# Kernel tuning notes

Measured on AMD Instinct MI355X. Metric: run time of the kernel, lower is better.

Reference implementation:

```python
import jax, jax.numpy as jnp
import numpy as np

B, N = 16, 4096

def _fps(xyz, npoint):
    # iterative farthest point sampling on one cloud [n,3] -> [npoint] int32
    n = xyz.shape[0]
    def body(carry, _):
        dist, far = carry
        d = jnp.sum((xyz - xyz[far]) ** 2, axis=-1)
        dist = jnp.minimum(dist, d)
        return (dist, jnp.argmax(dist).astype(jnp.int32)), far
    _, idx = jax.lax.scan(body, (jnp.full((n,), 1e10, jnp.float32), jnp.int32(0)), None, length=npoint)
    return idx

def _ball_query(radius, nsample, xyz, new_xyz):
    # xyz [n,3], new_xyz [S,3] -> [S,nsample] neighbor indices (first-in-index order, as in PointNet++)
    n = xyz.shape[0]
    sqr = jnp.sum((new_xyz[:, None, :] - xyz[None, :, :]) ** 2, axis=-1)  # [S,n]
    idx = jnp.where(sqr > radius * radius, n, jnp.arange(n, dtype=jnp.int32)[None, :])
    idx = jnp.sort(idx, axis=-1)[:, :nsample]
    return jnp.where(idx == n, idx[:, :1], idx)

def _gather(p, i):
    return jax.vmap(lambda pp, ii: pp[ii])(p, i)

def _mlp(x, layers):
    # shared MLP = 1x1 conv over grouped points; BN(eval) folded into (W,b)
    for W, b in layers:
        x = jax.nn.relu(jnp.einsum('bsnc,co->bsno', x, W) + b)
    return x

def _sa(xyz, feats, npoint, radius, nsample, layers):
    fps_idx = jax.vmap(lambda p: _fps(p, npoint))(xyz)            # [B,S]
    new_xyz = _gather(xyz, fps_idx)                                # [B,S,3]
    idx = jax.vmap(lambda p, q: _ball_query(radius, nsample, p, q))(xyz, new_xyz)  # [B,S,ns]
    x = _gather(xyz, idx) - new_xyz[:, :, None, :]                 # centered grouped xyz
    if feats is not None:
        x = jnp.concatenate([x, _gather(feats, idx)], axis=-1)
    x = _mlp(x, layers)
    return new_xyz, jnp.max(x, axis=2)

def _forward(points, w10, b10, w11, b11, w12, b12, w20, b20, w21, b21, w22, b22, w30, b30, w31, b31, w32, b32, lw1, lb1, lw2, lb2, fw1, fb1, fw2, fb2, pos_mean, pos_std, rot_mean, rot_std):
    l1x, l1f = _sa(points, None, 512, 0.2, 32, [(w10, b10), (w11, b11), (w12, b12)])
    l2x, l2f = _sa(l1x, l1f, 128, 0.4, 64, [(w20, b20), (w21, b21), (w22, b22)])
    # sa3: group_all
    x = jnp.concatenate([l2x, l2f], axis=-1)[:, None]              # [B,1,128,259]
    x = _mlp(x, [(w30, b30), (w31, b31), (w32, b32)])
    g = jnp.max(x, axis=2).reshape(points.shape[0], 1024)
    label = jax.nn.sigmoid(jax.nn.relu(g @ lw1 + lb1) @ lw2 + lb2)  # dropout = identity (eval)
    res = jax.nn.relu(g @ fw1 + fb1) @ fw2 + fb2
    pl = res[:, 0:3] * pos_std + pos_mean
    rl = res[:, 3:9] * rot_std + rot_mean
    pr = res[:, 9:12] * pos_std + pos_mean
    rr = res[:, 12:18] * rot_std + rot_mean
    return jnp.concatenate([label, pl, rl, pr, rr], axis=-1)       # [B,20]

def setup_inputs():
    ks = iter(jax.random.split(jax.random.key(0), 64))
    def w(shape, s=0.05):
        return jax.random.normal(next(ks), shape, jnp.float32) * s
    inp = {'points': jax.random.normal(next(ks), (B, N, 3), jnp.float32) * 0.5}
    dims = {'w10': (3, 64), 'w11': (64, 64), 'w12': (64, 128), 'w20': (131, 128), 'w21': (128, 128), 'w22': (128, 256), 'w30': (259, 256), 'w31': (256, 512), 'w32': (512, 1024), 'lw1': (1024, 256), 'lw2': (256, 2), 'fw1': (1024, 512), 'fw2': (512, 18)}
    for name, s in dims.items():
        inp[name] = w(s)
        inp[name.replace('w', 'b', 1)] = jnp.zeros((s[1],), jnp.float32)
    inp['pos_mean'] = w((3,), 0.1)
    inp['pos_std'] = jnp.abs(w((3,))) + 1.0
    inp['rot_mean'] = w((6,), 0.1)
    inp['rot_std'] = jnp.abs(w((6,))) + 1.0
    return inp

def reference(points, w10, b10, w11, b11, w12, b12, w20, b20, w21, b21, w22, b22, w30, b30, w31, b31, w32, b32, lw1, lb1, lw2, lb2, fw1, fb1, fw2, fb2, pos_mean, pos_std, rot_mean, rot_std):
    return _forward(points, w10, b10, w11, b11, w12, b12, w20, b20, w21, b21, w22, b22, w30, b30, w31, b31, w32, b32, lw1, lb1, lw2, lb2, fw1, fb1, fw2, fb2, pos_mean, pos_std, rot_mean, rot_std)
```

## Files before the change

### kernel.cpp

```cpp
#include <hip/hip_runtime.h>
#include <math.h>

#define BB 16
#define NN 4096

typedef float v2f __attribute__((ext_vector_type(2)));

__device__ __forceinline__ v2f pkfma(v2f a, v2f b, v2f c) {
    return __builtin_elementwise_fma(a, b, c);
}

__device__ __forceinline__ float sq3(float dx, float dy, float dz) {
    return __fadd_rn(__fadd_rn(__fmul_rn(dx, dx), __fmul_rn(dy, dy)), __fmul_rn(dz, dz));
}

template<int CTRL, int RMASK>
__device__ __forceinline__ unsigned long long dpp_max_step(unsigned long long P) {
    int lo = __builtin_amdgcn_update_dpp(0, (int)(unsigned)P,        CTRL, RMASK, 0xf, true);
    int hi = __builtin_amdgcn_update_dpp(0, (int)(unsigned)(P >> 32), CTRL, RMASK, 0xf, true);
    unsigned long long o = ((unsigned long long)(unsigned)hi << 32) | (unsigned)lo;
    return (o > P) ? o : P;
}

__device__ __forceinline__ unsigned long long dpp_wave_max_u64(unsigned long long P) {
    P = dpp_max_step<0x111, 0xf>(P);
    P = dpp_max_step<0x112, 0xf>(P);
    P = dpp_max_step<0x114, 0xf>(P);
    P = dpp_max_step<0x118, 0xf>(P);
    P = dpp_max_step<0x142, 0xa>(P);
    P = dpp_max_step<0x143, 0xc>(P);
    return P;
}

__device__ __forceinline__ unsigned long long u64max(unsigned long long a, unsigned long long b) {
    return (a > b) ? a : b;
}

template<int NPTS, int NPOINT, int TPB>
__global__ __launch_bounds__(TPB) void fps_kernel(const float* __restrict__ xyz,
                                                  float* __restrict__ newxyz,
                                                  float* __restrict__ out_t,
                                                  int ts) {
    constexpr int PPT = NPTS / TPB;
    constexpr int NW  = TPB / 64;
    static_assert(NPOINT <= TPB, "far-history latch needs NPOINT <= TPB");
    __shared__ float sx[NPTS], sy[NPTS], sz[NPTS];
    __shared__ __align__(16) unsigned long long slot[2][NW];
    const int b = blockIdx.x;
    const int tid = threadIdx.x;
    const float* base = xyz + (size_t)b * NPTS * 3;
    for (int i = tid; i < NPTS; i += TPB) {
        sx[i] = base[i * 3 + 0];
        sy[i] = base[i * 3 + 1];
        sz[i] = base[i * 3 + 2];
    }
    __syncthreads();
    float px[PPT], py[PPT], pz[PPT], dist[PPT];
#pragma unroll
    for (int k = 0; k < PPT; k++) {
        int p = tid + k * TPB;
        px[k] = sx[p]; py[k] = sy[p]; pz[k] = sz[p];
        dist[k] = 1e10f;
    }
    int far = 0;
    int myfar = 0;
    const int lane = tid & 63, wid = tid >> 6;
    for (int it = 0; it < NPOINT; it++) {
        if (tid == it) myfar = far;
        float fx = sx[far], fy = sy[far], fz = sz[far];
        float bv = -1.0f; int bi = 0;
#pragma unroll
        for (int k = 0; k < PPT; k++) {
            float d = sq3(px[k] - fx, py[k] - fy, pz[k] - fz);
            float nd = fminf(dist[k], d);
            dist[k] = nd;
            if (nd > bv) { bv = nd; bi = tid + k * TPB; }
        }
        unsigned long long P = ((unsigned long long)__float_as_uint(bv) << 32)
                             | (unsigned long long)(~(unsigned)bi & 0xFFFFFFFFull);
        P = dpp_wave_max_u64(P);
        int bufi = it & 1;
        if (lane == 63) slot[bufi][wid] = P;
        __syncthreads();
        unsigned long long v[NW];
#pragma unroll
        for (int w = 0; w < NW; w++) v[w] = slot[bufi][w];
#pragma unroll
        for (int st = NW / 2; st >= 1; st >>= 1)
#pragma unroll
            for (int w = 0; w < st; w++) v[w] = u64max(v[w], v[w + st]);
        far = (int)(~(unsigned)(v[0] & 0xFFFFFFFFull));
    }
    if (tid < NPOINT) {
        float fx = sx[myfar], fy = sy[myfar], fz = sz[myfar];
        newxyz[((size_t)b * NPOINT + tid) * 3 + 0] = fx;
        newxyz[((size_t)b * NPOINT + tid) * 3 + 1] = fy;
        newxyz[((size_t)b * NPOINT + tid) * 3 + 2] = fz;
        if (out_t) {
            out_t[0 * ts + b * NPOINT + tid] = fx;
            out_t[1 * ts + b * NPOINT + tid] = fy;
            out_t[2 * ts + b * NPOINT + tid] = fz;
        }
    }
}

template<int NS>
__device__ __forceinline__ void bq_body(const float* __restrict__ pts, int n,
                                        const float* __restrict__ centers, int S,
                                        float r2, int* __restrict__ outidx,
                                        int wave, int lane) {
    int b = wave / S, s = wave % S;
    const float* c = centers + ((size_t)b * S + s) * 3;
    float cx = c[0], cy = c[1], cz = c[2];
    const float* pb = pts + (size_t)b * n * 3;
    int* out = outidx + ((size_t)b * S + s) * NS;
    int total = 0, first = -1;
    int rounds = n >> 6;
    for (int r = 0; r < rounds; r++) {
        int p = (r << 6) + lane;
        float dx = pb[p * 3 + 0] - cx, dy = pb[p * 3 + 1] - cy, dz = pb[p * 3 + 2] - cz;
        float d = sq3(dx, dy, dz);
        bool pred = (d <= r2);
        unsigned long long mask = __ballot(pred);
        if (first < 0 && mask) first = (r << 6) + (__ffsll(mask) - 1);
        if (pred) {
            int rank = total + __popcll(mask & ((1ull << lane) - 1ull));
            if (rank < NS) out[rank] = p;
        }
        total += __popcll(mask);
        if (total >= NS) break;
    }
    for (int j = total + lane; j < NS; j += 64) out[j] = first;
}

__global__ __launch_bounds__(512) void bq1_fps2_kernel(const float* __restrict__ points,
                                                       const float* __restrict__ l1x,
                                                       float* __restrict__ l2x,
                                                       float* __restrict__ x3t,
                                                       int* __restrict__ idx1,
                                                       float r2a) {
    __shared__ float sx[512], sy[512], sz[512];
    const int tid = threadIdx.x;
    const int lane = tid & 63, wid = tid >> 6;
    if (blockIdx.x < 16) {
        if (wid != 0) return;
        const int b = blockIdx.x;
        const float* base = l1x + (size_t)b * 512 * 3;
        for (int i = lane; i < 512; i += 64) {
            sx[i] = base[i * 3 + 0];
            sy[i] = base[i * 3 + 1];
            sz[i] = base[i * 3 + 2];
        }
        float px[8], py[8], pz[8], dist[8];
#pragma unroll
        for (int k = 0; k < 8; k++) {
            int p = lane + k * 64;
            px[k] = sx[p]; py[k] = sy[p]; pz[k] = sz[p];
            dist[k] = 1e10f;
        }
        int far = 0, myfar0 = 0, myfar1 = 0;
        for (int it = 0; it < 128; it++) {
            if (lane == it) myfar0 = far;
            if (lane == it - 64) myfar1 = far;
            float fx = sx[far], fy = sy[far], fz = sz[far];
            float bv = -1.0f; int bi = 0;
#pragma unroll
            for (int k = 0; k < 8; k++) {
                float d = sq3(px[k] - fx, py[k] - fy, pz[k] - fz);
                float nd = fminf(dist[k], d);
                dist[k] = nd;
                if (nd > bv) { bv = nd; bi = lane + k * 64; }
            }
            unsigned long long P = ((unsigned long long)__float_as_uint(bv) << 32)
                                 | (unsigned long long)(~(unsigned)bi & 0xFFFFFFFFull);
            P = dpp_wave_max_u64(P);
            unsigned lo = (unsigned)__builtin_amdgcn_readlane((int)(unsigned)P, 63);
            far = (int)(~lo);
        }
        {
            int s0 = lane, s1 = lane + 64;
            float a = sx[myfar0], c1 = sy[myfar0], c2 = sz[myfar0];
            l2x[((size_t)b * 128 + s0) * 3 + 0] = a;
            l2x[((size_t)b * 128 + s0) * 3 + 1] = c1;
            l2x[((size_t)b * 128 + s0) * 3 + 2] = c2;
            x3t[0 * 2048 + b * 128 + s0] = a;
            x3t[1 * 2048 + b * 128 + s0] = c1;
            x3t[2 * 2048 + b * 128 + s0] = c2;
            float d = sx[myfar1], e = sy[myfar1], f = sz[myfar1];
            l2x[((size_t)b * 128 + s1) * 3 + 0] = d;
            l2x[((size_t)b * 128 + s1) * 3 + 1] = e;
            l2x[((size_t)b * 128 + s1) * 3 + 2] = f;
            x3t[0 * 2048 + b * 128 + s1] = d;
            x3t[1 * 2048 + b * 128 + s1] = e;
            x3t[2 * 2048 + b * 128 + s1] = f;
        }
    } else {
        int wave = (blockIdx.x - 16) * 8 + wid;
        bq_body<32>(points, 4096, l1x, 512, r2a, idx1, wave, lane);
    }
}

__global__ __launch_bounds__(64, 2) void sa1_bq2_kernel(const float* __restrict__ xyz, const float* __restrict__ l1x,
                                                 const int* __restrict__ idx1,
                                                 const float* __restrict__ l2x, int* __restrict__ idx2, float r2b,
                                                 const float* __restrict__ W1, const float* __restrict__ B1,
                                                 const float* __restrict__ W2, const float* __restrict__ B2,
                                                 const float* __restrict__ W3, const float* __restrict__ B3,
                                                 float* __restrict__ l1f) {
    __shared__ float ht[64 * 64];
    int lane = threadIdx.x;
    if (blockIdx.x < 2048) {
        bq_body<64>(l1x, 512, l2x, 128, r2b, idx2, blockIdx.x, lane);
        return;
    }
    int blk = blockIdx.x - 2048;
    int b = blk >> 8;
    int s = ((blk & 255) << 1) | (lane >> 5);
    int nn = lane & 31;
    int center = b * 512 + s;
    int ii = idx1[center * 32 + nn];
    float px = xyz[((size_t)b * NN + ii) * 3 + 0] - l1x[(size_t)center * 3 + 0];
    float py = xyz[((size_t)b * NN + ii) * 3 + 1] - l1x[(size_t)center * 3 + 1];
    float pz = xyz[((size_t)b * NN + ii) * 3 + 2] - l1x[(size_t)center * 3 + 2];
#pragma unroll
    for (int c = 0; c < 64; c++)
        ht[c * 64 + lane] = fmaxf(B1[c] + px * W1[c] + py * W1[64 + c] + pz * W1[128 + c], 0.0f);
    __syncthreads();
    v2f h2[32];
    const v2f* B2v = (const v2f*)B2;
#pragma unroll
    for (int c = 0; c < 32; c++) h2[c] = B2v[c];
    for (int k = 0; k < 64; k++) {
        float xk = ht[k * 64 + lane];
        v2f xk2 = {xk, xk};
        const v2f* wr = (const v2f*)(W2 + k * 64);
#pragma unroll
        for (int c = 0; c < 32; c++) h2[c] = pkfma(xk2, wr[c], h2[c]);
    }
    __syncthreads();
#pragma unroll
    for (int c = 0; c < 32; c++) {
        ht[(2 * c + 0) * 64 + lane] = fmaxf(h2[c].x, 0.0f);
        ht[(2 * c + 1) * 64 + lane] = fmaxf(h2[c].y, 0.0f);
    }
    __syncthreads();
#pragma unroll
    for (int half = 0; half < 2; half++) {
        v2f o[32];
        const v2f* B3v = (const v2f*)(B3 + half * 64);
#pragma unroll
        for (int j = 0; j < 32; j++) o[j] = B3v[j];
        for (int k = 0; k < 64; k++) {
            float xk = ht[k * 64 + lane];
            v2f xk2 = {xk, xk};
            const v2f* wr = (const v2f*)(W3 + k * 128 + half * 64);
#pragma unroll
            for (int j = 0; j < 32; j++) o[j] = pkfma(xk2, wr[j], o[j]);
        }
#pragma unroll
        for (int j = 0; j < 32; j++) {
            float va = fmaxf(o[j].x, 0.0f);
            float vb = fmaxf(o[j].y, 0.0f);
#pragma unroll
            for (int m = 16; m >= 1; m >>= 1) {
                va = fmaxf(va, __shfl_xor(va, m));
                vb = fmaxf(vb, __shfl_xor(vb, m));
            }
            o[j].x = va; o[j].y = vb;
        }
        if (nn == 0) {
#pragma unroll
            for (int j = 0; j < 32; j++) {
                l1f[(size_t)center * 128 + half * 64 + 2 * j + 0] = o[j].x;
                l1f[(size_t)center * 128 + half * 64 + 2 * j + 1] = o[j].y;
            }
        }
    }
}

__global__ __launch_bounds__(256, 4) void sa2_kernel(const float* __restrict__ l1x, const float* __restrict__ l2x,
                                                  const float* __restrict__ l1f, const int* __restrict__ idx2,
                                                  const float* __restrict__ W1, const float* __restrict__ B1,
                                                  const float* __restrict__ W2, const float* __restrict__ B2,
                                                  const float* __restrict__ W3, const float* __restrict__ B3,
                                                  float* __restrict__ x3t) {
    __shared__ float ht[128 * 64];
    int tid = threadIdx.x;
    int w = __builtin_amdgcn_readfirstlane(tid >> 6);
    int lane = tid & 63;
    int b = blockIdx.x >> 7, s = blockIdx.x & 127;
    int center = b * 128 + s;
    int ii = idx2[center * 64 + lane];
    float cx = l2x[(size_t)center * 3 + 0], cy = l2x[(size_t)center * 3 + 1], cz = l2x[(size_t)center * 3 + 2];
    const float* pr = l1x + ((size_t)b * 512 + ii) * 3;
    float px = pr[0] - cx, py = pr[1] - cy, pz = pr[2] - cz;
    const float4* frow = (const float4*)(l1f + ((size_t)b * 512 + ii) * 128);
    v2f h[16];
    {
        const v2f* B1v = (const v2f*)(B1 + w * 32);
        const v2f* w1a = (const v2f*)(W1 + 0 * 128 + w * 32);
        const v2f* w1b = (const v2f*)(W1 + 1 * 128 + w * 32);
        const v2f* w1c = (const v2f*)(W1 + 2 * 128 + w * 32);
        v2f px2 = {px, px}, py2 = {py, py}, pz2 = {pz, pz};
#pragma unroll
        for (int j = 0; j < 16; j++)
            h[j] = pkfma(pz2, w1c[j], pkfma(py2, w1b[j], pkfma(px2, w1a[j], B1v[j])));
    }
#pragma unroll 2
    for (int k4 = 0; k4 < 32; k4++) {
        float4 f = frow[k4];
        const v2f* wr = (const v2f*)(W1 + (3 + k4 * 4) * 128 + w * 32);
        v2f fx2 = {f.x, f.x}, fy2 = {f.y, f.y}, fz2 = {f.z, f.z}, fw2 = {f.w, f.w};
#pragma unroll
        for (int j = 0; j < 16; j++) {
            h[j] = pkfma(fx2, wr[j], h[j]);
            h[j] = pkfma(fy2, wr[64 + j], h[j]);
            h[j] = pkfma(fz2, wr[128 + j], h[j]);
            h[j] = pkfma(fw2, wr[192 + j], h[j]);
        }
    }
#pragma unroll
    for (int j = 0; j < 16; j++) {
        ht[(w * 32 + 2 * j + 0) * 64 + lane] = fmaxf(h[j].x, 0.0f);
        ht[(w * 32 + 2 * j + 1) * 64 + lane] = fmaxf(h[j].y, 0.0f);
    }
    __syncthreads();
    v2f h2[16];
    {
        const v2f* B2v = (const v2f*)(B2 + w * 32);
#pragma unroll
        for (int j = 0; j < 16; j++) h2[j] = B2v[j];
    }
#pragma unroll 2
    for (int k = 0; k < 128; k++) {
        float xk = ht[k * 64 + lane];
        v2f xk2 = {xk, xk};
        const v2f* wr = (const v2f*)(W2 + k * 128 + w * 32);
#pragma unroll
        for (int j = 0; j < 16; j++) h2[j] = pkfma(xk2, wr[j], h2[j]);
    }
    __syncthreads();
#pragma unroll
    for (int j = 0; j < 16; j++) {
        ht[(w * 32 + 2 * j + 0) * 64 + lane] = fmaxf(h2[j].x, 0.0f);
        ht[(w * 32 + 2 * j + 1) * 64 + lane] = fmaxf(h2[j].y, 0.0f);
    }
    __syncthreads();
#pragma unroll
    for (int half = 0; half < 2; half++) {
        v2f o[16];
        const v2f* B3v = (const v2f*)(B3 + w * 64 + half * 32);
#pragma unroll
        for (int j = 0; j < 16; j++) o[j] = B3v[j];
#pragma unroll 2
        for (int k = 0; k < 128; k++) {
            float xk = ht[k * 64 + lane];
            v2f xk2 = {xk, xk};
            const v2f* wr = (const v2f*)(W3 + k * 256 + w * 64 + half * 32);
#pragma unroll
            for (int j = 0; j < 16; j++) o[j] = pkfma(xk2, wr[j], o[j]);
        }
#pragma unroll
        for (int j = 0; j < 16; j++) {
            float va = fmaxf(o[j].x, 0.0f);
            float vb = fmaxf(o[j].y, 0.0f);
#pragma unroll
            for (int m = 32; m >= 1; m >>= 1) {
                va = fmaxf(va, __shfl_xor(va, m));
                vb = fmaxf(vb, __shfl_xor(vb, m));
            }
            o[j].x = va; o[j].y = vb;
        }
        if (lane == 0) {
#pragma unroll
            for (int j = 0; j < 16; j++) {
                x3t[(size_t)(3 + w * 64 + half * 32 + 2 * j + 0) * 2048 + center] = o[j].x;
                x3t[(size_t)(3 + w * 64 + half * 32 + 2 * j + 1) * 2048 + center] = o[j].y;
            }
        }
    }
}

template<int K, int COUT, int CPT, bool MAXOUT>
__device__ __forceinline__ void gemm_t_body(const float* __restrict__ in_t,
                                            const float* __restrict__ W,
                                            const float* __restrict__ bias,
                                            float* __restrict__ outp,
                                            int bid, int lane) {
    int rw = bid & 31, cg = bid >> 5;
    int row = rw * 64 + lane;
    int cbase = cg * CPT;
    v2f acc[CPT / 2];
    const v2f* bv = (const v2f*)(bias + cbase);
#pragma unroll
    for (int j = 0; j < CPT / 2; j++) acc[j] = bv[j];
    for (int k = 0; k < K; k++) {
        float xk = in_t[(size_t)k * 2048 + row];
        v2f xk2 = {xk, xk};
        const v2f* wr = (const v2f*)(W + (size_t)k * COUT + cbase);
#pragma unroll
        for (int j = 0; j < CPT / 2; j++) acc[j] = pkfma(xk2, wr[j], acc[j]);
    }
    if (MAXOUT) {
        int b = row >> 7;
#pragma unroll
        for (int j = 0; j < CPT / 2; j++) {
            float va = fmaxf(acc[j].x, 0.0f);
            float vb = fmaxf(acc[j].y, 0.0f);
#pragma unroll
            for (int m = 32; m >= 1; m >>= 1) {
                va = fmaxf(va, __shfl_xor(va, m));
                vb = fmaxf(vb, __shfl_xor(vb, m));
            }
            if (lane == 0) {
                atomicMax((int*)(outp + (size_t)b * 1024 + cbase + 2 * j + 0), __float_as_int(va));
                atomicMax((int*)(outp + (size_t)b * 1024 + cbase + 2 * j + 1), __float_as_int(vb));
            }
        }
    } else {
#pragma unroll
        for (int j = 0; j < CPT / 2; j++) {
            outp[(size_t)(cbase + 2 * j + 0) * 2048 + row] = fmaxf(acc[j].x, 0.0f);
            outp[(size_t)(cbase + 2 * j + 1) * 2048 + row] = fmaxf(acc[j].y, 0.0f);
        }
    }
}

template<int K, int COUT, int CPT, bool MAXOUT>
__global__ __launch_bounds__(64, 4) void gemm_t_kernel(const float* __restrict__ in_t,
                                                    const float* __restrict__ W,
                                                    const float* __restrict__ bias,
                                                    float* __restrict__ outp) {
    gemm_t_body<K, COUT, CPT, MAXOUT>(in_t, W, bias, outp, blockIdx.x, threadIdx.x);
}

__global__ __launch_bounds__(64, 4) void gemm1_zerog_kernel(const float* __restrict__ in_t,
                                                            const float* __restrict__ W,
                                                            const float* __restrict__ bias,
                                                            float* __restrict__ outp,
                                                            float* __restrict__ g) {
    if (blockIdx.x < 1024) {
        gemm_t_body<259, 256, 8, false>(in_t, W, bias, outp, blockIdx.x, threadIdx.x);
    } else {
        g[(blockIdx.x - 1024) * 64 + threadIdx.x] = 0.0f;
    }
}

__global__ __launch_bounds__(512) void head_kernel(const float* __restrict__ g,
                                                   const float* __restrict__ lw1, const float* __restrict__ lb1,
                                                   const float* __restrict__ lw2, const float* __restrict__ lb2,
                                                   const float* __restrict__ fw1, const float* __restrict__ fb1,
                                                   const float* __restrict__ fw2, const float* __restrict__ fb2,
                                                   const float* __restrict__ pm, const float* __restrict__ ps,
                                                   const float* __restrict__ rm, const float* __restrict__ rs,
                                                   float* __restrict__ out) {
    __shared__ float gl[1024], a1[256], f1[512];
    int b = blockIdx.x, t = threadIdx.x;
    for (int i = t; i < 1024; i += 512) gl[i] = g[b * 1024 + i];
    __syncthreads();
    {
        float acc = fb1[t];
        for (int k = 0; k < 1024; k++) acc += gl[k] * fw1[k * 512 + t];
        f1[t] = fmaxf(acc, 0.0f);
    }
    if (t < 256) {
        float acc = lb1[t];
        for (int k = 0; k < 1024; k++) acc += gl[k] * lw1[k * 256 + t];
        a1[t] = fmaxf(acc, 0.0f);
    }
    __syncthreads();
    if (t < 2) {
        float z = lb2[t];
        for (int k = 0; k < 256; k++) z += a1[k] * lw2[k * 2 + t];
        out[b * 20 + t] = 1.0f / (1.0f + expf(-z));
    } else if (t < 20) {
        int i = t - 2;
        float z = fb2[i];
        for (int k = 0; k < 512; k++) z += f1[k] * fw2[k * 18 + i];
        float sc, mn;
        if (i < 3)       { sc = ps[i];      mn = pm[i]; }
        else if (i < 9)  { sc = rs[i - 3];  mn = rm[i - 3]; }
        else if (i < 12) { sc = ps[i - 9];  mn = pm[i - 9]; }
        else             { sc = rs[i - 12]; mn = rm[i - 12]; }
        out[b * 20 + t] = z * sc + mn;
    }
}

static inline size_t align256(size_t x) { return (x + 255) & ~(size_t)255; }

extern "C" void kernel_launch(void* const* d_in, const int* in_sizes, int n_in,
                              void* d_out, int out_size, void* d_ws, size_t ws_size,
                              hipStream_t stream) {
    const float* points = (const float*)d_in[0];
    const float* w10 = (const float*)d_in[1];  const float* b10 = (const float*)d_in[2];
    const float* w11 = (const float*)d_in[3];  const float* b11 = (const float*)d_in[4];
    const float* w12 = (const float*)d_in[5];  const float* b12 = (const float*)d_in[6];
    const float* w20 = (const float*)d_in[7];  const float* b20 = (const float*)d_in[8];
    const float* w21 = (const float*)d_in[9];  const float* b21 = (const float*)d_in[10];
    const float* w22 = (const float*)d_in[11]; const float* b22 = (const float*)d_in[12];
    const float* w30 = (const float*)d_in[13]; const float* b30 = (const float*)d_in[14];
    const float* w31 = (const float*)d_in[15]; const float* b31 = (const float*)d_in[16];
    const float* w32 = (const float*)d_in[17]; const float* b32 = (const float*)d_in[18];
    const float* lw1 = (const float*)d_in[19]; const float* lb1 = (const float*)d_in[20];
    const float* lw2 = (const float*)d_in[21]; const float* lb2 = (const float*)d_in[22];
    const float* fw1 = (const float*)d_in[23]; const float* fb1 = (const float*)d_in[24];
    const float* fw2 = (const float*)d_in[25]; const float* fb2 = (const float*)d_in[26];
    const float* pm  = (const float*)d_in[27]; const float* ps  = (const float*)d_in[28];
    const float* rm  = (const float*)d_in[29]; const float* rs  = (const float*)d_in[30];
    float* out = (float*)d_out;

    char* p = (char*)d_ws;
    float* l1x  = (float*)p; p += align256((size_t)BB * 512 * 3 * 4);
    int*   idx1 = (int*)p;   p += align256((size_t)BB * 512 * 32 * 4);
    float* l1f  = (float*)p; p += align256((size_t)BB * 512 * 128 * 4);
    float* l2x  = (float*)p; p += align256((size_t)BB * 128 * 3 * 4);
    int*   idx2 = (int*)p;   p += align256((size_t)BB * 128 * 64 * 4);
    float* x3t  = (float*)p; p += align256((size_t)259 * 2048 * 4);
    float* h1t  = (float*)p; p += align256((size_t)256 * 2048 * 4);
    float* h2t  = (float*)p; p += align256((size_t)512 * 2048 * 4);
    float* g    = (float*)p; p += align256((size_t)BB * 1024 * 4);

    const float R2A = (float)(0.2 * 0.2);
    const float R2B = (float)(0.4 * 0.4);

    fps_kernel<4096, 512, 512><<<BB, 512, 0, stream>>>(points, l1x, (float*)nullptr, 0);
    bq1_fps2_kernel<<<1040, 512, 0, stream>>>(points, l1x, l2x, x3t, idx1, R2A);
    sa1_bq2_kernel<<<6144, 64, 0, stream>>>(points, l1x, idx1, l2x, idx2, R2B,
                                            w10, b10, w11, b11, w12, b12, l1f);
    sa2_kernel<<<2048, 256, 0, stream>>>(l1x, l2x, l1f, idx2, w20, b20, w21, b21, w22, b22, x3t);
    gemm1_zerog_kernel<<<1280, 64, 0, stream>>>(x3t, w30, b30, h1t, g);
    gemm_t_kernel<256, 512, 8, false><<<2048, 64, 0, stream>>>(h1t, w31, b31, h2t);
    gemm_t_kernel<512, 1024, 8, true><<<4096, 64, 0, stream>>>(h2t, w32, b32, g);
    head_kernel<<<BB, 512, 0, stream>>>(g, lw1, lb1, lw2, lb2, fw1, fb1, fw2, fb2, pm, ps, rm, rs, out);
}
```

Measured before the change: 954.6 us.

## Use split-bf16 MFMA for sa2 second and third MLP layers

Replaces the scalar packed-FMA loops for the 128->128 and 128->256 layers in sa2 with 16x16x32 bf16 MFMA. Three products per tile (hi*hi, hi*lo, lo*hi) keep accuracy close to fp32. Weights are pre-split into hi/lo bf16 fragment layout by extra blocks in the earlier bq1 kernel, written into the unused h1t buffer. Activations are staged in LDS as padded hi/lo bf16 rows. The intent is to move the dominant FLOPs onto matrix cores, at the cost of extra MFMAs for the split and a small rounding error versus fp32.

```diff
diff --git a/kernel.cpp b/kernel.cpp
--- a/kernel.cpp
+++ b/kernel.cpp
@@ -5,9 +5,25 @@
 #define NN 4096
 
 typedef float v2f __attribute__((ext_vector_type(2)));
+typedef short bfrag8 __attribute__((ext_vector_type(8)));
+typedef float fx4 __attribute__((ext_vector_type(4)));
 
 __device__ __forceinline__ v2f pkfma(v2f a, v2f b, v2f c) {
     return __builtin_elementwise_fma(a, b, c);
+}
+
+__device__ __forceinline__ fx4 mfma16(bfrag8 a, bfrag8 b, fx4 c) {
+    return __builtin_amdgcn_mfma_f32_16x16x32_bf16(a, b, c, 0, 0, 0);
+}
+
+__device__ __forceinline__ unsigned short bf16rne(float v) {
+    unsigned u = __float_as_uint(v);
+    return (unsigned short)((u + 0x7FFFu + ((u >> 16) & 1u)) >> 16);
+}
+__device__ __forceinline__ void bf16split(float v, unsigned short& h, unsigned short& l) {
+    h = bf16rne(v);
+    float fh = __uint_as_float((unsigned)h << 16);
+    l = bf16rne(v - fh);
 }
 
 __device__ __forceinline__ float sq3(float dx, float dy, float dz) {
@@ -138,7 +154,11 @@
                                                        float* __restrict__ l2x,
                                                        float* __restrict__ x3t,
                                                        int* __restrict__ idx1,
-                                                       float r2a) {
+                                                       float r2a,
+                                                       const float* __restrict__ w21,
+                                                       const float* __restrict__ w22,
+                                                       float* __restrict__ w21f,
+                                                       float* __restrict__ w22f) {
     __shared__ float sx[512], sy[512], sz[512];
     const int tid = threadIdx.x;
     const int lane = tid & 63, wid = tid >> 6;
@@ -194,9 +214,33 @@
             x3t[1 * 2048 + b * 128 + s1] = e;
             x3t[2 * 2048 + b * 128 + s1] = f;
         }
-    } else {
+    } else if (blockIdx.x < 1040) {
         int wave = (blockIdx.x - 16) * 8 + wid;
         bq_body<32>(points, 4096, l1x, 512, r2a, idx1, wave, lane);
+    } else {
+        int gt = (blockIdx.x - 1040) * 512 + tid;
+        const float* W; float* OF; int NT, N; int t;
+        if (gt < 4096) { W = w21; OF = w21f; NT = 8;  N = 128; t = gt; }
+        else           { W = w22; OF = w22f; NT = 16; N = 256; t = gt - 4096; }
+        int L = t & 63;
+        int rest = t >> 6;
+        int nt = rest & (NT - 1);
+        int hk = (NT == 8) ? (rest >> 3) : (rest >> 4);
+        int kt = hk & 3, hl = hk >> 2;
+        int k0 = kt * 32 + (L >> 4) * 8;
+        int n  = nt * 16 + (L & 15);
+        unsigned o[4];
+#pragma unroll
+        for (int e = 0; e < 4; e++) {
+            float va = W[(size_t)(k0 + 2 * e + 0) * N + n];
+            float vb = W[(size_t)(k0 + 2 * e + 1) * N + n];
+            unsigned short ha, la, hb, lb;
+            bf16split(va, ha, la);
+            bf16split(vb, hb, lb);
+            o[e] = hl ? ((unsigned)la | ((unsigned)lb << 16))
+                      : ((unsigned)ha | ((unsigned)hb << 16));
+        }
+        ((uint4*)OF)[t] = make_uint4(o[0], o[1], o[2], o[3]);
     }
 }
 
@@ -281,10 +325,11 @@
 __global__ __launch_bounds__(256, 4) void sa2_kernel(const float* __restrict__ l1x, const float* __restrict__ l2x,
                                                   const float* __restrict__ l1f, const int* __restrict__ idx2,
                                                   const float* __restrict__ W1, const float* __restrict__ B1,
-                                                  const float* __restrict__ W2, const float* __restrict__ B2,
-                                                  const float* __restrict__ W3, const float* __restrict__ B3,
+                                                  const float* __restrict__ w21f, const float* __restrict__ B2,
+                                                  const float* __restrict__ w22f, const float* __restrict__ B3,
                                                   float* __restrict__ x3t) {
-    __shared__ float ht[128 * 64];
+    __shared__ short hsh[64 * 136];
+    __shared__ short hsl[64 * 136];
     int tid = threadIdx.x;
     int w = __builtin_amdgcn_readfirstlane(tid >> 6);
     int lane = tid & 63;
@@ -321,62 +366,108 @@
     }
 #pragma unroll
     for (int j = 0; j < 16; j++) {
-        ht[(w * 32 + 2 * j + 0) * 64 + lane] = fmaxf(h[j].x, 0.0f);
-        ht[(w * 32 + 2 * j + 1) * 64 + lane] = fmaxf(h[j].y, 0.0f);
+        float v0 = fmaxf(h[j].x, 0.0f);
+        float v1 = fmaxf(h[j].y, 0.0f);
+        unsigned short h0, l0, h1, l1;
+        bf16split(v0, h0, l0);
+        bf16split(v1, h1, l1);
+        int cb = lane * 136 + w * 32 + 2 * j;
+        *(unsigned*)(&hsh[cb]) = (unsigned)h0 | ((unsigned)h1 << 16);
+        *(unsigned*)(&hsl[cb]) = (unsigned)l0 | ((unsigned)l1 << 16);
     }
     __syncthreads();
-    v2f h2[16];
     {
-        const v2f* B2v = (const v2f*)(B2 + w * 32);
-#pragma unroll
-        for (int j = 0; j < 16; j++) h2[j] = B2v[j];
-    }
-#pragma unroll 2
-    for (int k = 0; k < 128; k++) {
-        float xk = ht[k * 64 + lane];
-        v2f xk2 = {xk, xk};
-        const v2f* wr = (const v2f*)(W2 + k * 128 + w * 32);
-#pragma unroll
-        for (int j = 0; j < 16; j++) h2[j] = pkfma(xk2, wr[j], h2[j]);
-    }
-    __syncthreads();
-#pragma unroll
-    for (int j = 0; j < 16; j++) {
-        ht[(w * 32 + 2 * j + 0) * 64 + lane] = fmaxf(h2[j].x, 0.0f);
-        ht[(w * 32 + 2 * j + 1) * 64 + lane] = fmaxf(h2[j].y, 0.0f);
-    }
-    __syncthreads();
-#pragma unroll
-    for (int half = 0; half < 2; half++) {
-        v2f o[16];
-        const v2f* B3v = (const v2f*)(B3 + w * 64 + half * 32);
-#pragma unroll
-        for (int j = 0; j < 16; j++) o[j] = B3v[j];
-#pragma unroll 2
-        for (int k = 0; k < 128; k++) {
-            float xk = ht[k * 64 + lane];
-            v2f xk2 = {xk, xk};
-            const v2f* wr = (const v2f*)(W3 + k * 256 + w * 64 + half * 32);
-#pragma unroll
-            for (int j = 0; j < 16; j++) o[j] = pkfma(xk2, wr[j], o[j]);
-        }
-#pragma unroll
-        for (int j = 0; j < 16; j++) {
-            float va = fmaxf(o[j].x, 0.0f);
-            float vb = fmaxf(o[j].y, 0.0f);
-#pragma unroll
-            for (int m = 32; m >= 1; m >>= 1) {
-                va = fmaxf(va, __shfl_xor(va, m));
-                vb = fmaxf(vb, __shfl_xor(vb, m));
-            }
-            o[j].x = va; o[j].y = vb;
-        }
-        if (lane == 0) {
-#pragma unroll
-            for (int j = 0; j < 16; j++) {
-                x3t[(size_t)(3 + w * 64 + half * 32 + 2 * j + 0) * 2048 + center] = o[j].x;
-                x3t[(size_t)(3 + w * 64 + half * 32 + 2 * j + 1) * 2048 + center] = o[j].y;
-            }
+        fx4 acc[4][2];
+#pragma unroll
+        for (int mt = 0; mt < 4; mt++)
+#pragma unroll
+            for (int nt = 0; nt < 2; nt++) {
+                float bn = B2[(2 * w + nt) * 16 + (lane & 15)];
+                acc[mt][nt] = (fx4){bn, bn, bn, bn};
+            }
+#pragma unroll
+        for (int kt = 0; kt < 4; kt++) {
+            bfrag8 ah[4], al[4];
+#pragma unroll
+            for (int mt = 0; mt < 4; mt++) {
+                int idx = (mt * 16 + (lane & 15)) * 136 + kt * 32 + (lane >> 4) * 8;
+                ah[mt] = *(const bfrag8*)(&hsh[idx]);
+                al[mt] = *(const bfrag8*)(&hsl[idx]);
+            }
+#pragma unroll
+            for (int nt = 0; nt < 2; nt++) {
+                int ng = 2 * w + nt;
+                bfrag8 bh = ((const bfrag8*)w21f)[(size_t)((0 + kt) * 8 + ng) * 64 + lane];
+                bfrag8 bl = ((const bfrag8*)w21f)[(size_t)((4 + kt) * 8 + ng) * 64 + lane];
+#pragma unroll
+                for (int mt = 0; mt < 4; mt++) {
+                    acc[mt][nt] = mfma16(ah[mt], bh, acc[mt][nt]);
+                    acc[mt][nt] = mfma16(ah[mt], bl, acc[mt][nt]);
+                    acc[mt][nt] = mfma16(al[mt], bh, acc[mt][nt]);
+                }
+            }
+        }
+        __syncthreads();
+#pragma unroll
+        for (int mt = 0; mt < 4; mt++)
+#pragma unroll
+            for (int nt = 0; nt < 2; nt++)
+#pragma unroll
+                for (int r = 0; r < 4; r++) {
+                    float v = fmaxf(acc[mt][nt][r], 0.0f);
+                    int m = mt * 16 + (lane >> 4) * 4 + r;
+                    int n = (2 * w + nt) * 16 + (lane & 15);
+                    unsigned short hb, lb;
+                    bf16split(v, hb, lb);
+                    hsh[m * 136 + n] = (short)hb;
+                    hsl[m * 136 + n] = (short)lb;
+                }
+        __syncthreads();
+    }
+#pragma unroll 1
+    for (int pass = 0; pass < 2; pass++) {
+        int nb = w * 4 + pass * 2;
+        fx4 acc[4][2];
+#pragma unroll
+        for (int mt = 0; mt < 4; mt++)
+#pragma unroll
+            for (int nt = 0; nt < 2; nt++) {
+                float bn = B3[(nb + nt) * 16 + (lane & 15)];
+                acc[mt][nt] = (fx4){bn, bn, bn, bn};
+            }
+#pragma unroll
+        for (int kt = 0; kt < 4; kt++) {
+            bfrag8 ah[4], al[4];
+#pragma unroll
+            for (int mt = 0; mt < 4; mt++) {
+                int idx = (mt * 16 + (lane & 15)) * 136 + kt * 32 + (lane >> 4) * 8;
+                ah[mt] = *(const bfrag8*)(&hsh[idx]);
+                al[mt] = *(const bfrag8*)(&hsl[idx]);
+            }
+#pragma unroll
+            for (int nt = 0; nt < 2; nt++) {
+                bfrag8 bh = ((const bfrag8*)w22f)[(size_t)((0 + kt) * 16 + (nb + nt)) * 64 + lane];
+                bfrag8 bl = ((const bfrag8*)w22f)[(size_t)((4 + kt) * 16 + (nb + nt)) * 64 + lane];
+#pragma unroll
+                for (int mt = 0; mt < 4; mt++) {
+                    acc[mt][nt] = mfma16(ah[mt], bh, acc[mt][nt]);
+                    acc[mt][nt] = mfma16(ah[mt], bl, acc[mt][nt]);
+                    acc[mt][nt] = mfma16(al[mt], bh, acc[mt][nt]);
+                }
+            }
+        }
+#pragma unroll
+        for (int nt = 0; nt < 2; nt++) {
+            float mv = 0.0f;
+#pragma unroll
+            for (int mt = 0; mt < 4; mt++)
+#pragma unroll
+                for (int r = 0; r < 4; r++)
+                    mv = fmaxf(mv, acc[mt][nt][r]);
+            mv = fmaxf(mv, __shfl_xor(mv, 16));
+            mv = fmaxf(mv, __shfl_xor(mv, 32));
+            if (lane < 16)
+                x3t[(size_t)(3 + (nb + nt) * 16 + lane) * 2048 + center] = mv;
         }
     }
 }
@@ -519,15 +610,17 @@
     float* h1t  = (float*)p; p += align256((size_t)256 * 2048 * 4);
     float* h2t  = (float*)p; p += align256((size_t)512 * 2048 * 4);
     float* g    = (float*)p; p += align256((size_t)BB * 1024 * 4);
+    float* w21f = h1t;
+    float* w22f = h1t + (size_t)2 * 4 * 8 * 64 * 4;
 
     const float R2A = (float)(0.2 * 0.2);
     const float R2B = (float)(0.4 * 0.4);
 
     fps_kernel<4096, 512, 512><<<BB, 512, 0, stream>>>(points, l1x, (float*)nullptr, 0);
-    bq1_fps2_kernel<<<1040, 512, 0, stream>>>(points, l1x, l2x, x3t, idx1, R2A);
+    bq1_fps2_kernel<<<1064, 512, 0, stream>>>(points, l1x, l2x, x3t, idx1, R2A, w21, w22, w21f, w22f);
     sa1_bq2_kernel<<<6144, 64, 0, stream>>>(points, l1x, idx1, l2x, idx2, R2B,
                                             w10, b10, w11, b11, w12, b12, l1f);
-    sa2_kernel<<<2048, 256, 0, stream>>>(l1x, l2x, l1f, idx2, w20, b20, w21, b21, w22, b22, x3t);
+    sa2_kernel<<<2048, 256, 0, stream>>>(l1x, l2x, l1f, idx2, w20, b20, w21f, b21, w22f, b22, x3t);
     gemm1_zerog_kernel<<<1280, 64, 0, stream>>>(x3t, w30, b30, h1t, g);
     gemm_t_kernel<256, 512, 8, false><<<2048, 64, 0, stream>>>(h1t, w31, b31, h2t);
     gemm_t_kernel<512, 1024, 8, true><<<4096, 64, 0, stream>>>(h2t, w32, b32, g);
```

Result: faster. 922.4 us (-3.4%).
